# Kernel optimization log

Hardware: AMD Instinct MI355X
Metric: run time of the kernel (lower is better)

The kernel has to match this reference:

```python
import jax, jax.numpy as jnp
import numpy as np

B, LS, LL = 1024, 128, 2048
E, VOCAB = 16, 160000
NH, KD = 8, 6
LSH_DIM, TOPK = 16, 48
D_ITEM = 3 * E  # 48
EPS = 1e-3  # keras LayerNormalization default epsilon


def setup_inputs() -> dict:
    key = jax.random.key(0)
    ks = iter(jax.random.split(key, 64))
    def nk():
        return next(ks)
    def ids(shape):
        return jax.random.randint(nk(), shape, 0, VOCAB, dtype=jnp.int32)
    inp = {}
    for n in ['uid', 'utag1', 'utag2', 'utag3', 'utag4',
              'label_goods_ids', 'label_shop_ids', 'label_cate_ids']:
        inp[n] = ids((B,))
    for n in ['shortterm_goods_ids', 'shortterm_shop_ids', 'shortterm_cate_ids']:
        inp[n] = ids((B, LS))
    for n in ['longterm_goods_ids', 'longterm_shop_ids', 'longterm_cate_ids']:
        inp[n] = ids((B, LL))
    def rn(shape, s=0.05):
        return (jax.random.normal(nk(), shape) * s).astype(jnp.float32)
    inp['emb_table'] = rn((VOCAB, E))
    inp['H'] = rn((D_ITEM, LSH_DIM), 1.0)  # non-trainable random projection
    for p in ('s', 'l'):
        inp[p + 'Wq'] = rn((D_ITEM, NH, KD)); inp[p + 'bq'] = jnp.zeros((NH, KD), jnp.float32)
        inp[p + 'Wk'] = rn((D_ITEM, NH, KD)); inp[p + 'bk'] = jnp.zeros((NH, KD), jnp.float32)
        inp[p + 'Wv'] = rn((D_ITEM, NH, KD)); inp[p + 'bv'] = jnp.zeros((NH, KD), jnp.float32)
        inp[p + 'Wo'] = rn((NH, KD, D_ITEM)); inp[p + 'bo'] = jnp.zeros((D_ITEM,), jnp.float32)
    Din = D_ITEM + 5 * E + D_ITEM + D_ITEM  # 224
    inp['W1'] = rn((Din, 200)); inp['b1'] = jnp.zeros((200,), jnp.float32)
    inp['g1'] = jnp.ones((200,), jnp.float32); inp['be1'] = jnp.zeros((200,), jnp.float32)
    inp['W2'] = rn((200, 80)); inp['b2'] = jnp.zeros((80,), jnp.float32)
    inp['g2'] = jnp.ones((80,), jnp.float32); inp['be2'] = jnp.zeros((80,), jnp.float32)
    inp['W3'] = rn((80, 1)); inp['b3'] = jnp.zeros((1,), jnp.float32)
    return inp


def _ln(x, g, b):
    m = jnp.mean(x, axis=-1, keepdims=True)
    v = jnp.mean((x - m) ** 2, axis=-1, keepdims=True)
    return (x - m) * jax.lax.rsqrt(v + EPS) * g + b


def _mha(q, kv, mask3, Wq, bq, Wk, bk, Wv, bv, Wo, bo):
    # q: [B,1,D], kv: [B,K,D], mask3: [B,1,K] float (1=keep)
    qh = jnp.einsum('bqe,ehd->bqhd', q, Wq) + bq
    kh = jnp.einsum('bke,ehd->bkhd', kv, Wk) + bk
    vh = jnp.einsum('bke,ehd->bkhd', kv, Wv) + bv
    sc = jnp.einsum('bqhd,bkhd->bhqk', qh, kh) / jnp.sqrt(jnp.float32(KD))
    sc = sc + (1.0 - mask3[:, None, :, :]) * jnp.float32(-1e9)
    a = jax.nn.softmax(sc, axis=-1)
    o = jnp.einsum('bhqk,bkhd->bqhd', a, vh)
    return jnp.einsum('bqhd,hde->bqe', o, Wo) + bo


def reference(uid, utag1, utag2, utag3, utag4,
              label_goods_ids, label_shop_ids, label_cate_ids,
              shortterm_goods_ids, shortterm_shop_ids, shortterm_cate_ids,
              longterm_goods_ids, longterm_shop_ids, longterm_cate_ids,
              emb_table, H,
              sWq, sbq, sWk, sbk, sWv, sbv, sWo, sbo,
              lWq, lbq, lWk, lbk, lWv, lbv, lWo, lbo,
              W1, b1, g1, be1, W2, b2, g2, be2, W3, b3):
    short_mask = shortterm_goods_ids == 0  # padding_index == 0
    long_mask = longterm_goods_ids == 0

    def stack_embed(lst):
        X = jnp.stack([t if t.ndim == 2 else t[:, None] for t in lst], axis=2)  # [B,L,F]
        Xe = emb_table[X]  # [B,L,F,E]
        return Xe.reshape(Xe.shape[0], Xe.shape[1], -1)

    X_item = stack_embed([label_goods_ids, label_shop_ids, label_cate_ids])  # [B,1,48]
    X_user = stack_embed([uid, utag1, utag2, utag3, utag4])                  # [B,1,80]
    X_short = stack_embed([shortterm_goods_ids, shortterm_shop_ids, shortterm_cate_ids])  # [B,LS,48]
    X_long = stack_embed([longterm_goods_ids, longterm_shop_ids, longterm_cate_ids])      # [B,LL,48]

    # short-term interest
    slen = jnp.sum((~short_mask).astype(jnp.int32), axis=1)
    smask = (jnp.arange(LS)[None, :] < slen[:, None]).astype(jnp.float32)[:, None, :]
    short_int = _mha(X_item, X_short, smask, sWq, sbq, sWk, sbk, sWv, sbv, sWo, sbo)[:, 0]

    # long-term interest: LSH sign-hash hamming top-k retrieval
    series_codes = jnp.sign(jnp.einsum('ble,em->blm', X_long, H))  # [B,LL,16]
    item_codes = jnp.sign(jnp.einsum('ble,em->blm', X_item, H))    # [B,1,16]
    scores = jnp.sum((series_codes == item_codes).astype(jnp.float32), axis=-1)  # [B,LL]
    scores = jnp.where(long_mask, -jnp.inf, scores)
    _, idx = jax.lax.top_k(scores, TOPK)  # descending, padded entries last
    top_emb = jnp.take_along_axis(X_long, idx[:, :, None], axis=1)  # [B,TOPK,48]
    top_mask = jnp.take_along_axis(long_mask, idx, axis=1)
    llen = jnp.sum((~top_mask).astype(jnp.int32), axis=1)
    lmask = (jnp.arange(TOPK)[None, :] < llen[:, None]).astype(jnp.float32)[:, None, :]
    long_int = _mha(X_item, top_emb, lmask, lWq, lbq, lWk, lbk, lWv, lbv, lWo, lbo)[:, 0]

    x = jnp.concatenate([X_item[:, 0], X_user[:, 0], short_int, long_int], axis=1)  # [B,224]
    h1 = jax.nn.relu(_ln(x @ W1 + b1, g1, be1))
    h2 = jax.nn.relu(_ln(h1 @ W2 + b2, g2, be2))
    out = jax.nn.sigmoid(h2 @ W3 + b3)  # [B,1]
    return out
```

## Files before the change

kernel.cpp:

```cpp
#include <hip/hip_runtime.h>
#include <hip/hip_fp16.h>
#include <math.h>

#define BB 1024
#define LSx 128
#define LLx 2048
#define TOPKx 48
#define VOCABx 160000

__global__ __launch_bounds__(256) void k_partial(
    const float* __restrict__ emb, const float* __restrict__ Hm,
    __half* __restrict__ Ph)
{
  const int idx = blockIdx.x * 256 + threadIdx.x;
  if (idx >= VOCABx * 48) return;
  const int v = idx / 48;
  const int r = idx - v * 48;
  const int seg = r >> 4, m = r & 15;
  const float* er = emb + (size_t)v * 16;
  float a = 0.f;
  #pragma unroll
  for (int e = 0; e < 16; ++e) a += er[e] * Hm[(seg * 16 + e) * 16 + m];
  Ph[idx] = __float2half(a);
}

__global__ __launch_bounds__(512) void k_score_topk(
    const int* __restrict__ lg, const int* __restrict__ lsh, const int* __restrict__ lc,
    const int* __restrict__ ig, const int* __restrict__ ish, const int* __restrict__ ici,
    const float* __restrict__ emb, const float* __restrict__ Hm,
    const __half* __restrict__ Ph,
    int* __restrict__ sel)
{
  __shared__ int idsL[3 * LLx];
  __shared__ signed char scores[LLx];
  __shared__ float Xitem[48];
  __shared__ int icodeS[16];
  __shared__ int hist[18];
  __shared__ int cnt_above;
  __shared__ int wsum[8];
  const int b = blockIdx.x, tid = threadIdx.x;

  ((int4*)idsL)[tid]        = ((const int4*)(lg  + (size_t)b * LLx))[tid];
  ((int4*)idsL)[512 + tid]  = ((const int4*)(lsh + (size_t)b * LLx))[tid];
  ((int4*)idsL)[1024 + tid] = ((const int4*)(lc  + (size_t)b * LLx))[tid];
  if (tid < 48) {
    const int seg = tid >> 4, e = tid & 15;
    const int id = (seg == 0) ? ig[b] : (seg == 1) ? ish[b] : ici[b];
    Xitem[tid] = emb[(size_t)id * 16 + e];
  }
  if (tid < 18) hist[tid] = 0;
  if (tid == 0) cnt_above = 0;
  __syncthreads();
  if (tid < 16) {
    float dd = 0.f;
    for (int e = 0; e < 48; ++e) dd += Xitem[e] * Hm[e * 16 + tid];
    icodeS[tid] = (dd > 0.f) ? 1 : (dd < 0.f ? -1 : 0);
  }
  __syncthreads();

  const int l16 = tid & 15;
  const int grpw = (tid >> 4) & 3;
  const int grp32 = tid >> 4;
  const int myic = icodeS[l16];

  for (int r4 = 0; r4 < 64; r4 += 4) {
    int g_[4], s_[4], c_[4];
    #pragma unroll
    for (int u = 0; u < 4; ++u) {
      const int p = (r4 + u) * 32 + grp32;
      g_[u] = idsL[p]; s_[u] = idsL[LLx + p]; c_[u] = idsL[2 * LLx + p];
    }
    float d0[4], d1[4], d2[4];
    #pragma unroll
    for (int u = 0; u < 4; ++u) {
      d0[u] = __half2float(Ph[(size_t)g_[u] * 48 + l16]);
      d1[u] = __half2float(Ph[(size_t)s_[u] * 48 + 16 + l16]);
      d2[u] = __half2float(Ph[(size_t)c_[u] * 48 + 32 + l16]);
    }
    #pragma unroll
    for (int u = 0; u < 4; ++u) {
      const int p = (r4 + u) * 32 + grp32;
      const float d = (d0[u] + d1[u]) + d2[u];
      const int cs = (d > 0.f) ? 1 : (d < 0.f ? -1 : 0);
      const unsigned long long bal = __ballot(cs == myic);
      int sc = (int)__popcll((bal >> (16 * grpw)) & 0xFFFFull);
      if (g_[u] == 0) sc = -1;
      if (l16 == 0) {
        scores[p] = (signed char)sc;
        atomicAdd(&hist[sc + 1], 1);
      }
    }
  }
  __syncthreads();

  int above = 0, tval = -1, need = 0;
  for (int s = 16; s >= -1; --s) {
    const int c = hist[s + 1];
    if (above + c >= TOPKx) { tval = s; need = TOPKx - above; break; }
    above += c;
  }

  const int base_l = tid * 4;
  int myscore[4];
  #pragma unroll
  for (int j = 0; j < 4; ++j) myscore[j] = scores[base_l + j];
  int cnt = 0;
  #pragma unroll
  for (int j = 0; j < 4; ++j) cnt += (myscore[j] == tval) ? 1 : 0;
  int v = cnt;
  const int lane = tid & 63, wave = tid >> 6;
  #pragma unroll
  for (int o = 1; o < 64; o <<= 1) {
    const int u = __shfl_up(v, o, 64);
    if (lane >= o) v += u;
  }
  if (lane == 63) wsum[wave] = v;
  __syncthreads();
  int rank = v - cnt;
  for (int w = 0; w < wave; ++w) rank += wsum[w];

  #pragma unroll
  for (int j = 0; j < 4; ++j) {
    const int l = base_l + j;
    const int s = myscore[j];
    if (s > tval) {
      const int slot = atomicAdd(&cnt_above, 1);
      sel[b * TOPKx + slot] = l;
    } else if (s == tval) {
      if (rank < need) sel[b * TOPKx + above + rank] = l;
      ++rank;
    }
  }
}

__device__ __forceinline__ void kv_accum(
    const float* __restrict__ W, const float* __restrict__ bvec,
    int gid, int sid, int cid, const float* __restrict__ emb, float acc[48])
{
  #pragma unroll
  for (int j = 0; j < 48; ++j) acc[j] = bvec[j];
  const int ids3[3] = {gid, sid, cid};
  #pragma unroll
  for (int seg = 0; seg < 3; ++seg) {
    const float* row = emb + (size_t)ids3[seg] * 16;
    #pragma unroll
    for (int i4 = 0; i4 < 4; ++i4) {
      const float4 xv = ((const float4*)row)[i4];
      const float xs[4] = {xv.x, xv.y, xv.z, xv.w};
      #pragma unroll
      for (int c = 0; c < 4; ++c) {
        const int e = seg * 16 + i4 * 4 + c;
        const float* wr = W + e * 48;
        const float xe = xs[c];
        #pragma unroll
        for (int j = 0; j < 48; ++j) acc[j] += xe * wr[j];
      }
    }
  }
}

template<int K, int STRIDE, bool IS_LONG>
__global__ __launch_bounds__(256) void k_mha(
    const int* __restrict__ kg, const int* __restrict__ ks, const int* __restrict__ kc,
    const int* __restrict__ ig, const int* __restrict__ ish, const int* __restrict__ ici,
    const float* __restrict__ emb,
    const float* __restrict__ Wq, const float* __restrict__ bq,
    const float* __restrict__ Wk, const float* __restrict__ bk,
    const float* __restrict__ Wv, const float* __restrict__ bv,
    const float* __restrict__ Wo, const float* __restrict__ bo,
    const int* __restrict__ sel,
    float* __restrict__ outv)
{
  __shared__ float Xitem[48];
  __shared__ float qh[48];
  __shared__ __align__(16) float vhs[K][48];
  __shared__ float scs[8][K + 4];
  __shared__ float osm[48];
  __shared__ unsigned char validf[K];
  const int b = blockIdx.x, tid = threadIdx.x;
  const int role = tid >> 7;
  const int p = tid & 127;

  if (tid < 48) {
    const int seg = tid >> 4, e = tid & 15;
    const int id = (seg == 0) ? ig[b] : (seg == 1) ? ish[b] : ici[b];
    Xitem[tid] = emb[(size_t)id * 16 + e];
  }
  __syncthreads();
  if (tid < 48) {
    float a = bq[tid];
    for (int e = 0; e < 48; ++e) a += Xitem[e] * Wq[e * 48 + tid];
    qh[tid] = a;
  }

  int gid = 0, sid = 0, cid = 0;
  if (p < K) {
    const int pos = IS_LONG ? sel[b * TOPKx + p] : p;
    const size_t off = (size_t)b * STRIDE + pos;
    gid = kg[off]; sid = ks[off]; cid = kc[off];
  }
  const int nval = __syncthreads_count(role == 0 && p < K && gid != 0);

  if (p < K) {
    if (role == 0) {
      float acc[48];
      kv_accum(Wk, bk, gid, sid, cid, emb, acc);
      validf[p] = IS_LONG ? (unsigned char)(gid != 0) : (unsigned char)(p < nval);
      #pragma unroll
      for (int h = 0; h < 8; ++h) {
        float s = 0.f;
        #pragma unroll
        for (int d = 0; d < 6; ++d) s += qh[h * 6 + d] * acc[h * 6 + d];
        scs[h][p] = s * 0.40824829046386301637f;
      }
    } else {
      float acc[48];
      kv_accum(Wv, bv, gid, sid, cid, emb, acc);
      #pragma unroll
      for (int j = 0; j < 48; ++j) vhs[p][j] = acc[j];
    }
  }
  __syncthreads();

  if (tid < 128) {
    const int h = tid >> 4, l16 = tid & 15;
    float amax = -INFINITY;
    for (int k = l16; k < K; k += 16) if (validf[k]) amax = fmaxf(amax, scs[h][k]);
    #pragma unroll
    for (int m = 1; m < 16; m <<= 1) amax = fmaxf(amax, __shfl_xor(amax, m, 16));
    if (nval == 0) {
      for (int k = l16; k < K; k += 16) scs[h][k] = 1.0f / (float)K;
    } else {
      float ssum = 0.f;
      for (int k = l16; k < K; k += 16) {
        const float ev = validf[k] ? expf(scs[h][k] - amax) : 0.f;
        scs[h][k] = ev;
        ssum += ev;
      }
      #pragma unroll
      for (int m = 1; m < 16; m <<= 1) ssum += __shfl_xor(ssum, m, 16);
      const float inv = 1.0f / ssum;
      for (int k = l16; k < K; k += 16) scs[h][k] *= inv;
    }
  }
  __syncthreads();

  if (tid < 48) {
    const int h = tid / 6;
    float a = 0.f;
    for (int k = 0; k < K; ++k) a += scs[h][k] * vhs[k][tid];
    osm[tid] = a;
  }
  __syncthreads();
  if (tid < 48) {
    float r = bo[tid];
    for (int j = 0; j < 48; ++j) r += osm[j] * Wo[j * 48 + tid];
    outv[b * 48 + tid] = r;
  }
}

__device__ __forceinline__ float block_sum256(float v, float* red) {
  #pragma unroll
  for (int m = 32; m >= 1; m >>= 1) v += __shfl_xor(v, m, 64);
  const int lane = threadIdx.x & 63, wave = threadIdx.x >> 6;
  if (lane == 0) red[wave] = v;
  __syncthreads();
  const float t = red[0] + red[1] + red[2] + red[3];
  __syncthreads();
  return t;
}

__global__ __launch_bounds__(256) void k_mlp(
    const int* __restrict__ uid, const int* __restrict__ u1, const int* __restrict__ u2,
    const int* __restrict__ u3, const int* __restrict__ u4,
    const int* __restrict__ ig, const int* __restrict__ ish, const int* __restrict__ ici,
    const float* __restrict__ emb,
    const float* __restrict__ sint, const float* __restrict__ lint,
    const float* __restrict__ W1, const float* __restrict__ b1,
    const float* __restrict__ g1, const float* __restrict__ be1,
    const float* __restrict__ W2, const float* __restrict__ b2,
    const float* __restrict__ g2, const float* __restrict__ be2,
    const float* __restrict__ W3, const float* __restrict__ b3,
    float* __restrict__ out)
{
  __shared__ __align__(16) float x[224];
  __shared__ __align__(16) float h1[200];
  __shared__ float h2[80];
  __shared__ float red[4];
  const int b = blockIdx.x, tid = threadIdx.x;

  if (tid < 128) {
    const int e = tid & 15;
    int id;
    if (tid < 48) {
      const int seg = tid >> 4;
      id = (seg == 0) ? ig[b] : (seg == 1) ? ish[b] : ici[b];
    } else {
      const int f = (tid - 48) >> 4;
      id = (f == 0) ? uid[b] : (f == 1) ? u1[b] : (f == 2) ? u2[b] : (f == 3) ? u3[b] : u4[b];
    }
    x[tid] = emb[(size_t)id * 16 + e];
  } else if (tid < 176) {
    x[tid] = sint[b * 48 + (tid - 128)];
  } else if (tid < 224) {
    x[tid] = lint[b * 48 + (tid - 176)];
  }
  __syncthreads();

  float v = 0.f;
  if (tid < 200) {
    float a0 = b1[tid], a1 = 0.f, a2 = 0.f, a3 = 0.f;
    for (int i4 = 0; i4 < 56; ++i4) {
      const float4 xv = *(const float4*)(x + i4 * 4);
      const float* w = W1 + i4 * 4 * 200 + tid;
      a0 += xv.x * w[0];
      a1 += xv.y * w[200];
      a2 += xv.z * w[400];
      a3 += xv.w * w[600];
    }
    v = (a0 + a1) + (a2 + a3);
  }
  const float mean1 = block_sum256((tid < 200) ? v : 0.f, red) * (1.0f / 200.0f);
  const float dv = (tid < 200) ? (v - mean1) : 0.f;
  const float var1 = block_sum256(dv * dv, red) * (1.0f / 200.0f);
  if (tid < 200) {
    const float y = (v - mean1) * rsqrtf(var1 + 1e-3f) * g1[tid] + be1[tid];
    h1[tid] = fmaxf(y, 0.f);
  }
  __syncthreads();

  float v2 = 0.f;
  if (tid < 80) {
    float a0 = b2[tid], a1 = 0.f, a2 = 0.f, a3 = 0.f;
    for (int i4 = 0; i4 < 50; ++i4) {
      const float4 xv = *(const float4*)(h1 + i4 * 4);
      const float* w = W2 + i4 * 4 * 80 + tid;
      a0 += xv.x * w[0];
      a1 += xv.y * w[80];
      a2 += xv.z * w[160];
      a3 += xv.w * w[240];
    }
    v2 = (a0 + a1) + (a2 + a3);
  }
  const float mean2 = block_sum256((tid < 80) ? v2 : 0.f, red) * (1.0f / 80.0f);
  const float dv2 = (tid < 80) ? (v2 - mean2) : 0.f;
  const float var2 = block_sum256(dv2 * dv2, red) * (1.0f / 80.0f);
  if (tid < 80) {
    const float y = (v2 - mean2) * rsqrtf(var2 + 1e-3f) * g2[tid] + be2[tid];
    h2[tid] = fmaxf(y, 0.f);
  }
  __syncthreads();

  const float p = (tid < 80) ? h2[tid] * W3[tid] : 0.f;
  const float z = block_sum256(p, red);
  if (tid == 0) {
    out[b] = 1.0f / (1.0f + expf(-(z + b3[0])));
  }
}

extern "C" void kernel_launch(void* const* d_in, const int* in_sizes, int n_in,
                              void* d_out, int out_size, void* d_ws, size_t ws_size,
                              hipStream_t stream) {
  (void)in_sizes; (void)n_in; (void)out_size; (void)ws_size;
  const int* uid = (const int*)d_in[0];
  const int* u1  = (const int*)d_in[1];
  const int* u2  = (const int*)d_in[2];
  const int* u3  = (const int*)d_in[3];
  const int* u4  = (const int*)d_in[4];
  const int* ig  = (const int*)d_in[5];
  const int* ish = (const int*)d_in[6];
  const int* ici = (const int*)d_in[7];
  const int* sg  = (const int*)d_in[8];
  const int* ss  = (const int*)d_in[9];
  const int* scd = (const int*)d_in[10];
  const int* lg  = (const int*)d_in[11];
  const int* ls  = (const int*)d_in[12];
  const int* lcd = (const int*)d_in[13];
  const float* emb = (const float*)d_in[14];
  const float* Hm  = (const float*)d_in[15];
  const float* sWq = (const float*)d_in[16];
  const float* sbq = (const float*)d_in[17];
  const float* sWk = (const float*)d_in[18];
  const float* sbk = (const float*)d_in[19];
  const float* sWv = (const float*)d_in[20];
  const float* sbv = (const float*)d_in[21];
  const float* sWo = (const float*)d_in[22];
  const float* sbo = (const float*)d_in[23];
  const float* lWq = (const float*)d_in[24];
  const float* lbq = (const float*)d_in[25];
  const float* lWk = (const float*)d_in[26];
  const float* lbk = (const float*)d_in[27];
  const float* lWv = (const float*)d_in[28];
  const float* lbv = (const float*)d_in[29];
  const float* lWo = (const float*)d_in[30];
  const float* lbo = (const float*)d_in[31];
  const float* W1 = (const float*)d_in[32];
  const float* b1 = (const float*)d_in[33];
  const float* g1 = (const float*)d_in[34];
  const float* be1 = (const float*)d_in[35];
  const float* W2 = (const float*)d_in[36];
  const float* b2 = (const float*)d_in[37];
  const float* g2 = (const float*)d_in[38];
  const float* be2 = (const float*)d_in[39];
  const float* W3 = (const float*)d_in[40];
  const float* b3 = (const float*)d_in[41];
  float* out = (float*)d_out;

  int* sel = (int*)d_ws;
  float* sint = (float*)d_ws + BB * TOPKx;
  float* lint = sint + BB * 48;
  __half* Ph = (__half*)(lint + BB * 48);

  k_partial<<<dim3((VOCABx * 48 + 255) / 256), dim3(256), 0, stream>>>(emb, Hm, Ph);
  k_score_topk<<<dim3(BB), dim3(512), 0, stream>>>(lg, ls, lcd, ig, ish, ici, emb, Hm, Ph, sel);
  k_mha<128, 128, false><<<dim3(BB), dim3(256), 0, stream>>>(
      sg, ss, scd, ig, ish, ici, emb,
      sWq, sbq, sWk, sbk, sWv, sbv, sWo, sbo, (const int*)nullptr, sint);
  k_mha<48, 2048, true><<<dim3(BB), dim3(256), 0, stream>>>(
      lg, ls, lcd, ig, ish, ici, emb,
      lWq, lbq, lWk, lbk, lWv, lbv, lWo, lbo, sel, lint);
  k_mlp<<<dim3(BB), dim3(256), 0, stream>>>(
      uid, u1, u2, u3, u4, ig, ish, ici, emb,
      sint, lint, W1, b1, g1, be1, W2, b2, g2, be2, W3, b3, out);
}
```

Measured before the change: 342.5 us.

## Vectorize LSH partial table, deepen gather unroll, merge MHA kernels into one launch

k_partial now has each thread compute all 48 projections for one vocab row, load the embedding row as float4 and store packed half2 results as uint4. The score kernel unrolls its Ph gathers eight-deep to keep more loads in flight. The short and long attention kernels are merged into one 2*B-block launch with 128 threads, where each thread computes both the K and V projections for its key instead of splitting them across two thread halves. This removes a launch and redundant embedding reads but roughly doubles per-thread register pressure, and the shared pool is sized by hand.

```diff
diff --git a/kernel.cpp b/kernel.cpp
--- a/kernel.cpp
+++ b/kernel.cpp
@@ -12,16 +12,35 @@
     const float* __restrict__ emb, const float* __restrict__ Hm,
     __half* __restrict__ Ph)
 {
-  const int idx = blockIdx.x * 256 + threadIdx.x;
-  if (idx >= VOCABx * 48) return;
-  const int v = idx / 48;
-  const int r = idx - v * 48;
-  const int seg = r >> 4, m = r & 15;
-  const float* er = emb + (size_t)v * 16;
-  float a = 0.f;
-  #pragma unroll
-  for (int e = 0; e < 16; ++e) a += er[e] * Hm[(seg * 16 + e) * 16 + m];
-  Ph[idx] = __float2half(a);
+  const int v = blockIdx.x * 256 + threadIdx.x;
+  if (v >= VOCABx) return;
+  const float4* er = (const float4*)(emb + (size_t)v * 16);
+  const float4 x0 = er[0], x1 = er[1], x2 = er[2], x3 = er[3];
+  const float x[16] = {x0.x, x0.y, x0.z, x0.w, x1.x, x1.y, x1.z, x1.w,
+                       x2.x, x2.y, x2.z, x2.w, x3.x, x3.y, x3.z, x3.w};
+  unsigned int packed[24];
+  #pragma unroll
+  for (int seg = 0; seg < 3; ++seg) {
+    #pragma unroll
+    for (int mp = 0; mp < 8; ++mp) {
+      float a0 = 0.f, a1 = 0.f;
+      #pragma unroll
+      for (int e = 0; e < 16; ++e) {
+        a0 += x[e] * Hm[(seg * 16 + e) * 16 + 2 * mp];
+        a1 += x[e] * Hm[(seg * 16 + e) * 16 + 2 * mp + 1];
+      }
+      const __half2 hp = __floats2half2_rn(a0, a1);
+      packed[seg * 8 + mp] = *(const unsigned int*)&hp;
+    }
+  }
+  uint4* dst = (uint4*)(Ph + (size_t)v * 48);
+  #pragma unroll
+  for (int q = 0; q < 6; ++q) {
+    uint4 o;
+    o.x = packed[q * 4 + 0]; o.y = packed[q * 4 + 1];
+    o.z = packed[q * 4 + 2]; o.w = packed[q * 4 + 3];
+    dst[q] = o;
+  }
 }
 
 __global__ __launch_bounds__(512) void k_score_topk(
@@ -39,6 +58,7 @@
   __shared__ int cnt_above;
   __shared__ int wsum[8];
   const int b = blockIdx.x, tid = threadIdx.x;
+  const int lane = tid & 63, wave = tid >> 6;
 
   ((int4*)idsL)[tid]        = ((const int4*)(lg  + (size_t)b * LLx))[tid];
   ((int4*)idsL)[512 + tid]  = ((const int4*)(lsh + (size_t)b * LLx))[tid];
@@ -63,23 +83,23 @@
   const int grp32 = tid >> 4;
   const int myic = icodeS[l16];
 
-  for (int r4 = 0; r4 < 64; r4 += 4) {
-    int g_[4], s_[4], c_[4];
-    #pragma unroll
-    for (int u = 0; u < 4; ++u) {
-      const int p = (r4 + u) * 32 + grp32;
+  for (int r8 = 0; r8 < 64; r8 += 8) {
+    int g_[8], s_[8], c_[8];
+    #pragma unroll
+    for (int u = 0; u < 8; ++u) {
+      const int p = (r8 + u) * 32 + grp32;
       g_[u] = idsL[p]; s_[u] = idsL[LLx + p]; c_[u] = idsL[2 * LLx + p];
     }
-    float d0[4], d1[4], d2[4];
-    #pragma unroll
-    for (int u = 0; u < 4; ++u) {
+    float d0[8], d1[8], d2[8];
+    #pragma unroll
+    for (int u = 0; u < 8; ++u) {
       d0[u] = __half2float(Ph[(size_t)g_[u] * 48 + l16]);
       d1[u] = __half2float(Ph[(size_t)s_[u] * 48 + 16 + l16]);
       d2[u] = __half2float(Ph[(size_t)c_[u] * 48 + 32 + l16]);
     }
     #pragma unroll
-    for (int u = 0; u < 4; ++u) {
-      const int p = (r4 + u) * 32 + grp32;
+    for (int u = 0; u < 8; ++u) {
+      const int p = (r8 + u) * 32 + grp32;
       const float d = (d0[u] + d1[u]) + d2[u];
       const int cs = (d > 0.f) ? 1 : (d < 0.f ? -1 : 0);
       const unsigned long long bal = __ballot(cs == myic);
@@ -108,7 +128,6 @@
   #pragma unroll
   for (int j = 0; j < 4; ++j) cnt += (myscore[j] == tval) ? 1 : 0;
   int v = cnt;
-  const int lane = tid & 63, wave = tid >> 6;
   #pragma unroll
   for (int o = 1; o < 64; o <<= 1) {
     const int u = __shfl_up(v, o, 64);
@@ -133,34 +152,9 @@
   }
 }
 
-__device__ __forceinline__ void kv_accum(
-    const float* __restrict__ W, const float* __restrict__ bvec,
-    int gid, int sid, int cid, const float* __restrict__ emb, float acc[48])
-{
-  #pragma unroll
-  for (int j = 0; j < 48; ++j) acc[j] = bvec[j];
-  const int ids3[3] = {gid, sid, cid};
-  #pragma unroll
-  for (int seg = 0; seg < 3; ++seg) {
-    const float* row = emb + (size_t)ids3[seg] * 16;
-    #pragma unroll
-    for (int i4 = 0; i4 < 4; ++i4) {
-      const float4 xv = ((const float4*)row)[i4];
-      const float xs[4] = {xv.x, xv.y, xv.z, xv.w};
-      #pragma unroll
-      for (int c = 0; c < 4; ++c) {
-        const int e = seg * 16 + i4 * 4 + c;
-        const float* wr = W + e * 48;
-        const float xe = xs[c];
-        #pragma unroll
-        for (int j = 0; j < 48; ++j) acc[j] += xe * wr[j];
-      }
-    }
-  }
-}
-
 template<int K, int STRIDE, bool IS_LONG>
-__global__ __launch_bounds__(256) void k_mha(
+__device__ __forceinline__ void mha_body(
+    int b, char* pool,
     const int* __restrict__ kg, const int* __restrict__ ks, const int* __restrict__ kc,
     const int* __restrict__ ig, const int* __restrict__ ish, const int* __restrict__ ici,
     const float* __restrict__ emb,
@@ -171,15 +165,13 @@
     const int* __restrict__ sel,
     float* __restrict__ outv)
 {
-  __shared__ float Xitem[48];
-  __shared__ float qh[48];
-  __shared__ __align__(16) float vhs[K][48];
-  __shared__ float scs[8][K + 4];
-  __shared__ float osm[48];
-  __shared__ unsigned char validf[K];
-  const int b = blockIdx.x, tid = threadIdx.x;
-  const int role = tid >> 7;
-  const int p = tid & 127;
+  float* vhs = (float*)pool;
+  float* scs = (float*)(pool + K * 48 * 4);
+  float* Xitem = (float*)(pool + K * 48 * 4 + 8 * (K + 4) * 4);
+  float* qh = Xitem + 48;
+  float* osm = qh + 48;
+  unsigned char* validf = (unsigned char*)(osm + 48);
+  const int tid = threadIdx.x;
 
   if (tid < 48) {
     const int seg = tid >> 4, e = tid & 15;
@@ -194,53 +186,71 @@
   }
 
   int gid = 0, sid = 0, cid = 0;
-  if (p < K) {
-    const int pos = IS_LONG ? sel[b * TOPKx + p] : p;
+  if (tid < K) {
+    const int pos = IS_LONG ? sel[b * TOPKx + tid] : tid;
     const size_t off = (size_t)b * STRIDE + pos;
     gid = kg[off]; sid = ks[off]; cid = kc[off];
   }
-  const int nval = __syncthreads_count(role == 0 && p < K && gid != 0);
-
-  if (p < K) {
-    if (role == 0) {
-      float acc[48];
-      kv_accum(Wk, bk, gid, sid, cid, emb, acc);
-      validf[p] = IS_LONG ? (unsigned char)(gid != 0) : (unsigned char)(p < nval);
+  const int nval = __syncthreads_count((tid < K) && (gid != 0));
+
+  if (tid < K) {
+    validf[tid] = IS_LONG ? (unsigned char)(gid != 0) : (unsigned char)(tid < nval);
+    float kh[48], vh[48];
+    #pragma unroll
+    for (int j = 0; j < 48; ++j) { kh[j] = bk[j]; vh[j] = bv[j]; }
+    const int ids3[3] = {gid, sid, cid};
+    #pragma unroll
+    for (int seg = 0; seg < 3; ++seg) {
+      const float* row = emb + (size_t)ids3[seg] * 16;
       #pragma unroll
-      for (int h = 0; h < 8; ++h) {
-        float s = 0.f;
+      for (int i4 = 0; i4 < 4; ++i4) {
+        const float4 xv = ((const float4*)row)[i4];
+        const float xs[4] = {xv.x, xv.y, xv.z, xv.w};
         #pragma unroll
-        for (int d = 0; d < 6; ++d) s += qh[h * 6 + d] * acc[h * 6 + d];
-        scs[h][p] = s * 0.40824829046386301637f;
+        for (int c = 0; c < 4; ++c) {
+          const int e = seg * 16 + i4 * 4 + c;
+          const float* wkr = Wk + e * 48;
+          const float* wvr = Wv + e * 48;
+          const float xe = xs[c];
+          #pragma unroll
+          for (int j = 0; j < 48; ++j) {
+            kh[j] += xe * wkr[j];
+            vh[j] += xe * wvr[j];
+          }
+        }
       }
-    } else {
-      float acc[48];
-      kv_accum(Wv, bv, gid, sid, cid, emb, acc);
+    }
+    #pragma unroll
+    for (int h = 0; h < 8; ++h) {
+      float s = 0.f;
       #pragma unroll
-      for (int j = 0; j < 48; ++j) vhs[p][j] = acc[j];
-    }
-  }
-  __syncthreads();
-
-  if (tid < 128) {
+      for (int d = 0; d < 6; ++d) s += qh[h * 6 + d] * kh[h * 6 + d];
+      scs[h * (K + 4) + tid] = s * 0.40824829046386301637f;
+    }
+    #pragma unroll
+    for (int j = 0; j < 48; ++j) vhs[tid * 48 + j] = vh[j];
+  }
+  __syncthreads();
+
+  {
     const int h = tid >> 4, l16 = tid & 15;
     float amax = -INFINITY;
-    for (int k = l16; k < K; k += 16) if (validf[k]) amax = fmaxf(amax, scs[h][k]);
+    for (int k = l16; k < K; k += 16) if (validf[k]) amax = fmaxf(amax, scs[h * (K + 4) + k]);
     #pragma unroll
     for (int m = 1; m < 16; m <<= 1) amax = fmaxf(amax, __shfl_xor(amax, m, 16));
     if (nval == 0) {
-      for (int k = l16; k < K; k += 16) scs[h][k] = 1.0f / (float)K;
+      for (int k = l16; k < K; k += 16) scs[h * (K + 4) + k] = 1.0f / (float)K;
     } else {
       float ssum = 0.f;
       for (int k = l16; k < K; k += 16) {
-        const float ev = validf[k] ? expf(scs[h][k] - amax) : 0.f;
-        scs[h][k] = ev;
+        const float ev = validf[k] ? expf(scs[h * (K + 4) + k] - amax) : 0.f;
+        scs[h * (K + 4) + k] = ev;
         ssum += ev;
       }
       #pragma unroll
       for (int m = 1; m < 16; m <<= 1) ssum += __shfl_xor(ssum, m, 16);
       const float inv = 1.0f / ssum;
-      for (int k = l16; k < K; k += 16) scs[h][k] *= inv;
+      for (int k = l16; k < K; k += 16) scs[h * (K + 4) + k] *= inv;
     }
   }
   __syncthreads();
@@ -248,7 +258,7 @@
   if (tid < 48) {
     const int h = tid / 6;
     float a = 0.f;
-    for (int k = 0; k < K; ++k) a += scs[h][k] * vhs[k][tid];
+    for (int k = 0; k < K; ++k) a += scs[h * (K + 4) + k] * vhs[k * 48 + tid];
     osm[tid] = a;
   }
   __syncthreads();
@@ -256,6 +266,35 @@
     float r = bo[tid];
     for (int j = 0; j < 48; ++j) r += osm[j] * Wo[j * 48 + tid];
     outv[b * 48 + tid] = r;
+  }
+}
+
+__global__ __launch_bounds__(128) void k_mha_all(
+    const int* __restrict__ sg, const int* __restrict__ ss, const int* __restrict__ scd,
+    const int* __restrict__ lg, const int* __restrict__ ls, const int* __restrict__ lcd,
+    const int* __restrict__ ig, const int* __restrict__ ish, const int* __restrict__ ici,
+    const float* __restrict__ emb,
+    const float* __restrict__ sWq, const float* __restrict__ sbq,
+    const float* __restrict__ sWk, const float* __restrict__ sbk,
+    const float* __restrict__ sWv, const float* __restrict__ sbv,
+    const float* __restrict__ sWo, const float* __restrict__ sbo,
+    const float* __restrict__ lWq, const float* __restrict__ lbq,
+    const float* __restrict__ lWk, const float* __restrict__ lbk,
+    const float* __restrict__ lWv, const float* __restrict__ lbv,
+    const float* __restrict__ lWo, const float* __restrict__ lbo,
+    const int* __restrict__ sel,
+    float* __restrict__ sint, float* __restrict__ lint)
+{
+  __shared__ __align__(16) char pool[29888];
+  const int bid = blockIdx.x;
+  if (bid < BB) {
+    mha_body<LSx, LSx, false>(bid, pool, sg, ss, scd, ig, ish, ici, emb,
+                              sWq, sbq, sWk, sbk, sWv, sbv, sWo, sbo,
+                              (const int*)nullptr, sint);
+  } else {
+    mha_body<TOPKx, LLx, true>(bid - BB, pool, lg, ls, lcd, ig, ish, ici, emb,
+                               lWq, lbq, lWk, lbk, lWv, lbv, lWo, lbo,
+                               sel, lint);
   }
 }
 
@@ -411,14 +450,13 @@
   float* lint = sint + BB * 48;
   __half* Ph = (__half*)(lint + BB * 48);
 
-  k_partial<<<dim3((VOCABx * 48 + 255) / 256), dim3(256), 0, stream>>>(emb, Hm, Ph);
+  k_partial<<<dim3((VOCABx + 255) / 256), dim3(256), 0, stream>>>(emb, Hm, Ph);
   k_score_topk<<<dim3(BB), dim3(512), 0, stream>>>(lg, ls, lcd, ig, ish, ici, emb, Hm, Ph, sel);
-  k_mha<128, 128, false><<<dim3(BB), dim3(256), 0, stream>>>(
-      sg, ss, scd, ig, ish, ici, emb,
-      sWq, sbq, sWk, sbk, sWv, sbv, sWo, sbo, (const int*)nullptr, sint);
-  k_mha<48, 2048, true><<<dim3(BB), dim3(256), 0, stream>>>(
-      lg, ls, lcd, ig, ish, ici, emb,
-      lWq, lbq, lWk, lbk, lWv, lbv, lWo, lbo, sel, lint);
+  k_mha_all<<<dim3(2 * BB), dim3(128), 0, stream>>>(
+      sg, ss, scd, lg, ls, lcd, ig, ish, ici, emb,
+      sWq, sbq, sWk, sbk, sWv, sbv, sWo, sbo,
+      lWq, lbq, lWk, lbk, lWv, lbv, lWo, lbo,
+      sel, sint, lint);
   k_mlp<<<dim3(BB), dim3(256), 0, stream>>>(
       uid, u1, u2, u3, u4, ig, ish, ici, emb,
       sint, lint, W1, b1, g1, be1, W2, b2, g2, be2, W3, b3, out);
```

Result: no change. 336.3 us (-1.8%).
